# Optimization experiments

Hardware: AMD Instinct MI355X
Metric: run time of the kernel (lower is better)

Reference implementation:

```python
import jax, jax.numpy as jnp
import numpy as np

VOCAB = 32000      # embedding vocab
EMBED = 300        # nn.Embedding embedding_dim
HID = 256          # sequence_size // 2 per direction (sequence_size=512)
N_COLS = 4096      # number of columns (split-delimited segments)
SEG_LEN = 8        # 7 description words + 1 SPLIT token per column
SPLIT_IDX = 0
T = N_COLS * SEG_LEN


def setup_inputs() -> dict:
    key = jax.random.key(0)
    ks = jax.random.split(key, 10)
    # tokens in [1, VOCAB), with SPLIT_IDX at the end of every SEG_LEN block
    seq = jax.random.randint(ks[0], (T,), 1, VOCAB)
    seq = seq.at[SEG_LEN - 1::SEG_LEN].set(SPLIT_IDX)
    s = 1.0 / np.sqrt(HID)  # torch LSTM default init range

    def u(k, shape):
        return jax.random.uniform(k, shape, jnp.float32, -s, s)

    return {
        "emb_table": jax.random.normal(ks[1], (VOCAB, EMBED), jnp.float32),
        "w_ih_f": u(ks[2], (4 * HID, EMBED)),
        "w_hh_f": u(ks[3], (4 * HID, HID)),
        "b_ih_f": u(ks[4], (4 * HID,)),
        "b_hh_f": u(ks[5], (4 * HID,)),
        "w_ih_b": u(ks[6], (4 * HID, EMBED)),
        "w_hh_b": u(ks[7], (4 * HID, HID)),
        "b_ih_b": u(ks[8], (4 * HID,)),
        "b_hh_b": u(ks[9], (4 * HID,)),
        "seq_s": seq,
    }


def _run_dir(xg, mask, w_hh, reverse):
    """Masked LSTM over time. xg: [L, N, 4H] precomputed input gates (+bias),
    mask: [L, N] validity per original time index. Returns final hidden [N, H]."""
    if reverse:
        xg = xg[::-1]
        mask = mask[::-1]
    N = xg.shape[1]

    def step(carry, inp):
        h, c = carry
        g, m = inp
        gates = g + h @ w_hh.T                       # [N, 4H]
        i, f, gg, o = jnp.split(gates, 4, axis=-1)   # torch gate order i,f,g,o
        c_new = jax.nn.sigmoid(f) * c + jax.nn.sigmoid(i) * jnp.tanh(gg)
        h_new = jax.nn.sigmoid(o) * jnp.tanh(c_new)
        m = m[:, None]
        return (jnp.where(m, h_new, h), jnp.where(m, c_new, c)), None

    init = (jnp.zeros((N, HID), xg.dtype), jnp.zeros((N, HID), xg.dtype))
    (h, _), _ = jax.lax.scan(step, init, (xg, mask))
    return h


def reference(emb_table, w_ih_f, w_hh_f, b_ih_f, b_hh_f,
              w_ih_b, w_hh_b, b_ih_b, b_hh_b, seq_s):
    col = jnp.arange(N_COLS)
    # torch code: ends = nonzero(split); begins = roll(ends,1); begins[0] = 0
    # => segment i>0 starts AT the previous split token (len SEG_LEN);
    #    segment 0 is [0, SEG_LEN-1) (len SEG_LEN-1).
    begins = jnp.where(col == 0, 0, col * SEG_LEN - 1)
    lengths = jnp.where(col == 0, SEG_LEN - 1, SEG_LEN)
    idx = jnp.clip(begins[:, None] + jnp.arange(SEG_LEN)[None, :], 0, T - 1)  # [N, L]
    mask = jnp.arange(SEG_LEN)[None, :] < lengths[:, None]                    # [N, L]

    segs = emb_table[seq_s][idx]        # [N, L, E] embedded ragged segments
    x = segs.transpose(1, 0, 2)          # [L, N, E]
    m = mask.T                           # [L, N]

    xg_f = jnp.einsum('lne,ge->lng', x, w_ih_f) + b_ih_f + b_hh_f
    xg_b = jnp.einsum('lne,ge->lng', x, w_ih_b) + b_ih_b + b_hh_b
    h_f = _run_dir(xg_f, m, w_hh_f, reverse=False)   # forward final hidden
    h_b = _run_dir(xg_b, m, w_hh_b, reverse=True)    # backward final hidden (t=0)
    # torch final_hidden.view(-1) per column == concat(fwd, bwd)
    return jnp.concatenate([h_f, h_b], axis=-1)      # [N_COLS, 2*HID]
```

## Files before the change

kernel.cpp:

```cpp
#include <hip/hip_runtime.h>

typedef unsigned int uint;
typedef unsigned short ushort;
typedef __attribute__((ext_vector_type(8))) short short8;
typedef __attribute__((ext_vector_type(4))) float f32x4;
typedef __attribute__((ext_vector_type(4))) uint uint4w;

#define T_LEN 32768
#define EMB 300
#define HID 256
#define NCOLS 4096

__device__ __forceinline__ ushort f2bf(float f) {
  uint u = __float_as_uint(f);
  return (ushort)((u + 0x7fffu + ((u >> 16) & 1u)) >> 16);
}
__device__ __forceinline__ float bf2f(ushort u) {
  return __uint_as_float(((uint)u) << 16);
}
__device__ __forceinline__ float fexp2(float x) {
  float r; asm("v_exp_f32 %0, %1" : "=v"(r) : "v"(x)); return r;
}
__device__ __forceinline__ float frcp(float x) {
  float r; asm("v_rcp_f32 %0, %1" : "=v"(r) : "v"(x)); return r;
}
__device__ __forceinline__ float sigm(float x) {
  return frcp(1.f + fexp2(-1.442695041f * x));
}
__device__ __forceinline__ float tanh_(float x) {
  return 2.f * frcp(1.f + fexp2(-2.885390082f * x)) - 1.f;
}

__device__ __forceinline__ void gload_lds16(const void* g, void* l) {
  __builtin_amdgcn_global_load_lds((const __attribute__((address_space(1))) void*)g,
                                   (__attribute__((address_space(3))) void*)l, 16, 0, 0);
}

__global__ void prep_kernel(const float* __restrict__ emb,
                            const float* __restrict__ wihf, const float* __restrict__ whhf,
                            const float* __restrict__ bihf, const float* __restrict__ bhhf,
                            const float* __restrict__ wihb, const float* __restrict__ whhb,
                            const float* __restrict__ bihb, const float* __restrict__ bhhb,
                            const int* __restrict__ seq,
                            ushort* __restrict__ X, ushort* __restrict__ Wih,
                            ushort* __restrict__ Whh3, float* __restrict__ bias) {
  const int NX = T_LEN * 40;
  const int NWIH = 2048 * 40;
  const int NWHH = 2048 * 32;
  const int NB = 2048;
  const int total = NX + NWIH + NWHH + NB;
  for (int t = blockIdx.x * blockDim.x + threadIdx.x; t < total; t += gridDim.x * blockDim.x) {
    if (t < NX) {
      int r = t / 40, k8 = t % 40, k = k8 * 8;
      int col = r >> 3, j = r & 7;
      int tok = (col == 0) ? j : (col * 8 - 1 + j);
      const float* src = emb + (long)seq[tok] * EMB + k;
      alignas(16) ushort tmp[8];
#pragma unroll
      for (int i = 0; i < 8; ++i) tmp[i] = (k + i < EMB) ? f2bf(src[i]) : (ushort)0;
      *(uint4w*)(X + (long)r * 320 + k) = *(const uint4w*)tmp;
    } else if (t < NX + NWIH) {
      int t2 = t - NX;
      int n = t2 / 40, k8 = t2 % 40, k = k8 * 8;
      const float* src = ((n < 1024) ? wihf : wihb) + (long)(n & 1023) * EMB + k;
      alignas(16) ushort tmp[8];
#pragma unroll
      for (int i = 0; i < 8; ++i) tmp[i] = (k + i < EMB) ? f2bf(src[i]) : (ushort)0;
      *(uint4w*)(Wih + (long)n * 320 + k) = *(const uint4w*)tmp;
    } else if (t < NX + NWIH + NWHH) {
      int t3 = t - NX - NWIH;
      int n = t3 / 32, k8 = t3 % 32;
      int dd = n >> 10, rowg = n & 1023;
      int gp = rowg >> 9, gi = (rowg >> 8) & 1, w5 = (rowg >> 5) & 7;
      int qq = (rowg >> 4) & 1, lnn = rowg & 15;
      int ks = k8 >> 2, cc = k8 & 3, s = ks * 2 + gp;
      const float* src = ((dd == 0) ? whhf : whhb) + (long)rowg * HID + k8 * 8;
      alignas(16) ushort tmp[8];
#pragma unroll
      for (int i = 0; i < 8; ++i) tmp[i] = f2bf(src[i]);
      long didx = (((long)(dd * 16 + s)) * 8 + w5) * 2048 + cc * 512 + gi * 256 + qq * 128 + lnn * 8;
      *(uint4w*)(Whh3 + didx) = *(const uint4w*)tmp;
    } else {
      int n = t - NX - NWIH - NWHH;
      bias[n] = (n < 1024) ? (bihf[n] + bhhf[n]) : (bihb[n - 1024] + bhhb[n - 1024]);
    }
  }
}

__global__ void gemm_xg_kernel(const ushort* __restrict__ X, const ushort* __restrict__ Wih,
                               const float* __restrict__ bias, ushort* __restrict__ xg) {
  __shared__ ushort a_lds[2][256 * 32];
  const int tid = threadIdx.x;
  const int lane = tid & 63, w = tid >> 6;
  const int wr = w >> 1, wc = w & 1;
  const int qrow = lane >> 4, ln = lane & 15;
  const int m0 = blockIdx.x * 256, n0 = blockIdx.y * 128;

  auto stage = [&](int buf, int kt) {
#pragma unroll
    for (int q = 0; q < 2; ++q) {
      int byteoff = w * 2048 + q * 1024 + lane * 16;
      int row = byteoff >> 6, koff = byteoff & 63;
      const char* src = (const char*)X + (long)(m0 + row) * 640 + kt * 64 + koff;
      void* dst = (char*)&a_lds[buf][0] + w * 2048 + q * 1024;
      gload_lds16(src, dst);
    }
  };

  const ushort* wb = Wih + (long)(n0 + wc * 64 + ln) * 320 + qrow * 8;
  auto loadB = [&](short8 (&dst)[4], int kt) {
#pragma unroll
    for (int nt = 0; nt < 4; ++nt)
      dst[nt] = *(const short8*)(wb + nt * 16 * 320 + kt * 32);
  };

  const f32x4 fzero = {0.f, 0.f, 0.f, 0.f};
  f32x4 acc[4][4];
#pragma unroll
  for (int i = 0; i < 4; ++i)
#pragma unroll
    for (int jj = 0; jj < 4; ++jj) acc[i][jj] = fzero;

  auto gemmK = [&](short8 (&b)[4], int buf) {
    short8 a[4];
#pragma unroll
    for (int rt = 0; rt < 4; ++rt)
      a[rt] = *(const short8*)&a_lds[buf][(wr * 64 + rt * 16 + ln) * 32 + qrow * 8];
#pragma unroll
    for (int rt = 0; rt < 4; ++rt)
#pragma unroll
      for (int nt = 0; nt < 4; ++nt)
        acc[rt][nt] = __builtin_amdgcn_mfma_f32_16x16x32_bf16(a[rt], b[nt], acc[rt][nt], 0, 0, 0);
  };

  short8 bA[4], bB[4];
  stage(0, 0);
  loadB(bA, 0);
#pragma unroll 1
  for (int kt2 = 0; kt2 < 5; ++kt2) {
    const int kt = kt2 * 2;
    __syncthreads();
    loadB(bB, kt + 1);
    __builtin_amdgcn_sched_barrier(0);
    if (kt < 9) stage(1, kt + 1);
    __builtin_amdgcn_sched_barrier(0);
    gemmK(bA, 0);
    __syncthreads();
    if (kt2 < 4) loadB(bA, kt + 2);
    __builtin_amdgcn_sched_barrier(0);
    if (kt + 2 < 10) stage(0, kt + 2);
    __builtin_amdgcn_sched_barrier(0);
    gemmK(bB, 1);
  }

  ushort* sbuf = &a_lds[0][0];
  float bv[4];
#pragma unroll
  for (int nt = 0; nt < 4; ++nt) bv[nt] = bias[n0 + wc * 64 + nt * 16 + ln];
#pragma unroll
  for (int R = 0; R < 4; ++R) {
    __syncthreads();
#pragma unroll
    for (int nt = 0; nt < 4; ++nt)
#pragma unroll
      for (int r = 0; r < 4; ++r)
        sbuf[(wr * 16 + qrow * 4 + r) * 128 + wc * 64 + nt * 16 + ln] = f2bf(acc[R][nt][r] + bv[nt]);
    __syncthreads();
#pragma unroll
    for (int p = 0; p < 2; ++p) {
      int srow = p * 32 + (tid >> 4);
      int c0 = (tid & 15) * 8;
      uint4w v = *(uint4w*)&sbuf[srow * 128 + c0];
      *(uint4w*)&xg[(long)(m0 + (srow >> 4) * 64 + R * 16 + (srow & 15)) * 2048 + n0 + c0] = v;
    }
  }
}

__global__ __launch_bounds__(512) void lstm_kernel(const ushort* __restrict__ xg,
                                                   const ushort* __restrict__ Whh3,
                                                   float* __restrict__ out) {
  __shared__ ushort h_lds[32][264];
  __shared__ alignas(16) char b_lds[8][4][4096];
  const int tid = threadIdx.x;
  const int lane = tid & 63, w = tid >> 6;
  const int qrow = lane >> 4, ln = lane & 15;
  const int bid = blockIdx.x;
  const int d = bid >> 7, cg = bid & 127;

  const char* wsrc = (const char*)Whh3 + (((long)(d * 16) * 8 + w) << 12);
  char* wdst = &b_lds[w][0][0];

  auto stageB = [&](int s, int slot) {
    const char* src = wsrc + ((long)s << 15) + lane * 16;
    char* dst = wdst + slot * 4096;
#pragma unroll
    for (int q2 = 0; q2 < 4; ++q2) gload_lds16(src + q2 * 1024, dst + q2 * 1024);
  };

  float c_st[2][2][4], h_st[2][2][4];
#pragma unroll
  for (int rt = 0; rt < 2; ++rt)
#pragma unroll
    for (int q = 0; q < 2; ++q)
#pragma unroll
      for (int r = 0; r < 4; ++r) { c_st[rt][q][r] = 0.f; h_st[rt][q][r] = 0.f; }

  const f32x4 fzero = {0.f, 0.f, 0.f, 0.f};

#pragma unroll 1
  for (int it = 0; it < 8; ++it) {
    const int j = d ? (7 - it) : it;
    asm volatile("s_waitcnt lgkmcnt(0)" ::: "memory");
    __builtin_amdgcn_s_barrier();
    asm volatile("" ::: "memory");

    f32x4 acc[4][2][2];
#pragma unroll
    for (int g = 0; g < 4; ++g)
#pragma unroll
      for (int q = 0; q < 2; ++q)
#pragma unroll
        for (int rt = 0; rt < 2; ++rt) acc[g][q][rt] = fzero;

    if (it > 0) {
      asm volatile("s_waitcnt vmcnt(4)" ::: "memory");
      __builtin_amdgcn_sched_barrier(0);
      short8 bbuf[2][4], abuf[2][2];
      {
        const char* bb = wdst + qrow * 1024;
#pragma unroll
        for (int gi = 0; gi < 2; ++gi)
#pragma unroll
          for (int q = 0; q < 2; ++q)
            bbuf[0][gi * 2 + q] = *(const short8*)(bb + gi * 512 + q * 256 + ln * 16);
        abuf[0][0] = *(const short8*)&h_lds[ln][qrow * 8];
        abuf[0][1] = *(const short8*)&h_lds[16 + ln][qrow * 8];
      }
#pragma unroll
      for (int p = 0; p < 16; ++p) {
        const int ks = p >> 1, gp = p & 1;
        if (p < 15) {
          const char* bb = wdst + ((p + 1) & 3) * 4096 + qrow * 1024;
#pragma unroll
          for (int gi = 0; gi < 2; ++gi)
#pragma unroll
            for (int q = 0; q < 2; ++q)
              bbuf[(p + 1) & 1][gi * 2 + q] = *(const short8*)(bb + gi * 512 + q * 256 + ln * 16);
        }
        if (gp == 1 && ks < 7) {
          abuf[(ks + 1) & 1][0] = *(const short8*)&h_lds[ln][(ks + 1) * 32 + qrow * 8];
          abuf[(ks + 1) & 1][1] = *(const short8*)&h_lds[16 + ln][(ks + 1) * 32 + qrow * 8];
        }
        if (p <= 12) stageB(p + 3, (p + 3) & 3);
        if (p == 15)                 { asm volatile("s_waitcnt lgkmcnt(0)" ::: "memory"); }
        else if (gp == 1 && ks < 7)  { asm volatile("s_waitcnt lgkmcnt(6)" ::: "memory"); }
        else                         { asm volatile("s_waitcnt lgkmcnt(4)" ::: "memory"); }
        __builtin_amdgcn_sched_barrier(0);
        short8 a0 = abuf[ks & 1][0], a1 = abuf[ks & 1][1];
#pragma unroll
        for (int gi = 0; gi < 2; ++gi)
#pragma unroll
          for (int q = 0; q < 2; ++q) {
            short8 b = bbuf[p & 1][gi * 2 + q];
            const int g = gp * 2 + gi;
            acc[g][q][0] = __builtin_amdgcn_mfma_f32_16x16x32_bf16(a0, b, acc[g][q][0], 0, 0, 0);
            acc[g][q][1] = __builtin_amdgcn_mfma_f32_16x16x32_bf16(a1, b, acc[g][q][1], 0, 0, 0);
          }
        if (p < 15) { asm volatile("s_waitcnt vmcnt(4)" ::: "memory"); }
        __builtin_amdgcn_sched_barrier(0);
      }
    }

    if (it < 7) { stageB(0, 0); stageB(1, 1); stageB(2, 2); }
    __builtin_amdgcn_sched_barrier(0);

    const ushort* xgb = xg + (long)(cg * 256 + j) * 2048 + qrow * 65536 + d * 1024 + w * 32 + ln;
    ushort xv[2][2][4][4];
#pragma unroll
    for (int rt = 0; rt < 2; ++rt)
#pragma unroll
      for (int q = 0; q < 2; ++q)
#pragma unroll
        for (int r = 0; r < 4; ++r)
#pragma unroll
          for (int g = 0; g < 4; ++g)
            xv[rt][q][r][g] = xgb[(long)rt * 262144 + r * 16384 + g * 256 + q * 16];

    asm volatile("s_waitcnt lgkmcnt(0)" ::: "memory");
    __builtin_amdgcn_s_barrier();
    asm volatile("" ::: "memory");

    const bool mstep = d ? (it == 0) : (it == 7);
#pragma unroll
    for (int rt = 0; rt < 2; ++rt)
#pragma unroll
      for (int q = 0; q < 2; ++q)
#pragma unroll
        for (int r = 0; r < 4; ++r) {
          int cc = rt * 16 + qrow * 4 + r;
          int hid = w * 32 + q * 16 + ln;
          float pi = acc[0][q][rt][r] + bf2f(xv[rt][q][r][0]);
          float pf = acc[1][q][rt][r] + bf2f(xv[rt][q][r][1]);
          float pg = acc[2][q][rt][r] + bf2f(xv[rt][q][r][2]);
          float po = acc[3][q][rt][r] + bf2f(xv[rt][q][r][3]);
          float cn = sigm(pf) * c_st[rt][q][r] + sigm(pi) * tanh_(pg);
          float hn = sigm(po) * tanh_(cn);
          bool skip = mstep && (cg == 0) && (cc == 0);
          if (!skip) { c_st[rt][q][r] = cn; h_st[rt][q][r] = hn; }
          h_lds[cc][hid] = f2bf(h_st[rt][q][r]);
        }
  }

#pragma unroll
  for (int rt = 0; rt < 2; ++rt)
#pragma unroll
    for (int q = 0; q < 2; ++q)
#pragma unroll
      for (int r = 0; r < 4; ++r) {
        int cc = rt * 16 + qrow * 4 + r;
        int hid = w * 32 + q * 16 + ln;
        out[(long)(cg * 32 + cc) * 512 + d * 256 + hid] = h_st[rt][q][r];
      }
}

extern "C" void kernel_launch(void* const* d_in, const int* in_sizes, int n_in,
                              void* d_out, int out_size, void* d_ws, size_t ws_size,
                              hipStream_t stream) {
  const float* emb  = (const float*)d_in[0];
  const float* wihf = (const float*)d_in[1];
  const float* whhf = (const float*)d_in[2];
  const float* bihf = (const float*)d_in[3];
  const float* bhhf = (const float*)d_in[4];
  const float* wihb = (const float*)d_in[5];
  const float* whhb = (const float*)d_in[6];
  const float* bihb = (const float*)d_in[7];
  const float* bhhb = (const float*)d_in[8];
  const int*   seq  = (const int*)d_in[9];
  float* out = (float*)d_out;

  char* ws = (char*)d_ws;
  ushort* xg   = (ushort*)(ws);
  ushort* X    = (ushort*)(ws + 134217728);
  ushort* Wih  = (ushort*)(ws + 155189248);
  ushort* Whh3 = (ushort*)(ws + 156499968);
  float*  bias = (float*)(ws + 157548544);

  prep_kernel<<<dim3(1024), dim3(256), 0, stream>>>(emb, wihf, whhf, bihf, bhhf,
                                                    wihb, whhb, bihb, bhhb, seq,
                                                    X, Wih, Whh3, bias);
  gemm_xg_kernel<<<dim3(128, 16), dim3(512), 0, stream>>>(X, Wih, bias, xg);
  lstm_kernel<<<dim3(256), dim3(512), 0, stream>>>(xg, Whh3, out);
}
```

Before: 239.0 us.

## Restructure input-projection GEMM into triple-buffered B pipeline with single barrier per step

The input-gate GEMM's K loop is fully unrolled. B fragments are rotated through three register buffers so loads run two steps ahead, and each step uses one explicit s_barrier guarded by explicit lgkmcnt/vmcnt waits, replacing two __syncthreads per pair of steps. This aims to overlap global loads of B and LDS staging of A with the MFMA work and to cut barrier overhead. In the recurrent kernel, the tail vmcnt waits are also adjusted so the last iterations drain outstanding loads correctly. The cost is higher register pressure and reliance on hand-counted wait values being right.

```diff
diff --git a/kernel.cpp b/kernel.cpp
--- a/kernel.cpp
+++ b/kernel.cpp
@@ -133,24 +133,21 @@
         acc[rt][nt] = __builtin_amdgcn_mfma_f32_16x16x32_bf16(a[rt], b[nt], acc[rt][nt], 0, 0, 0);
   };
 
-  short8 bA[4], bB[4];
+  short8 b[3][4];
+  loadB(b[0], 0);
   stage(0, 0);
-  loadB(bA, 0);
-#pragma unroll 1
-  for (int kt2 = 0; kt2 < 5; ++kt2) {
-    const int kt = kt2 * 2;
-    __syncthreads();
-    loadB(bB, kt + 1);
+  loadB(b[1], 1);
+#pragma unroll
+  for (int kt = 0; kt < 10; ++kt) {
+    asm volatile("s_waitcnt lgkmcnt(0)" ::: "memory");
+    if (kt < 9) { asm volatile("s_waitcnt vmcnt(4)" ::: "memory"); }
+    else        { asm volatile("s_waitcnt vmcnt(0)" ::: "memory"); }
+    __builtin_amdgcn_s_barrier();
+    asm volatile("" ::: "memory");
+    if (kt < 9) stage((kt + 1) & 1, kt + 1);
+    if (kt < 8) loadB(b[(kt + 2) % 3], kt + 2);
     __builtin_amdgcn_sched_barrier(0);
-    if (kt < 9) stage(1, kt + 1);
-    __builtin_amdgcn_sched_barrier(0);
-    gemmK(bA, 0);
-    __syncthreads();
-    if (kt2 < 4) loadB(bA, kt + 2);
-    __builtin_amdgcn_sched_barrier(0);
-    if (kt + 2 < 10) stage(0, kt + 2);
-    __builtin_amdgcn_sched_barrier(0);
-    gemmK(bB, 1);
+    gemmK(b[kt % 3], kt & 1);
   }
 
   ushort* sbuf = &a_lds[0][0];
@@ -266,7 +263,8 @@
             acc[g][q][0] = __builtin_amdgcn_mfma_f32_16x16x32_bf16(a0, b, acc[g][q][0], 0, 0, 0);
             acc[g][q][1] = __builtin_amdgcn_mfma_f32_16x16x32_bf16(a1, b, acc[g][q][1], 0, 0, 0);
           }
-        if (p < 15) { asm volatile("s_waitcnt vmcnt(4)" ::: "memory"); }
+        if (p <= 12)      { asm volatile("s_waitcnt vmcnt(4)" ::: "memory"); }
+        else if (p == 13) { asm volatile("s_waitcnt vmcnt(0)" ::: "memory"); }
         __builtin_amdgcn_sched_barrier(0);
       }
     }
```

Result: slower. 355.4 us (+48.7%).

## Retile input-gate GEMM to 64x256 blocks of 256 threads and fix LSTM waitcnt tail

Applied to the files above, without the earlier changes.

Reshapes the input-projection GEMM from 256x128 tiles with 8 waves to 64x256 tiles with 4 waves, each wave covering a 64x64 output patch. The shared A buffer shrinks and launch bounds ask for 3 blocks per CU, aiming for higher occupancy and more blocks across CUs, at the cost of reloading the X rows more times per output column. The epilogue now writes 256-wide rows with two 16-byte stores per thread. In the LSTM kernel the vmcnt wait at the end of the pipelined loop is changed to drain fully at p==13 and skip waits afterwards, matching the point where staging stops.

```diff
diff --git a/kernel.cpp b/kernel.cpp
--- a/kernel.cpp
+++ b/kernel.cpp
@@ -87,27 +87,24 @@
   }
 }
 
-__global__ void gemm_xg_kernel(const ushort* __restrict__ X, const ushort* __restrict__ Wih,
-                               const float* __restrict__ bias, ushort* __restrict__ xg) {
-  __shared__ ushort a_lds[2][256 * 32];
+__global__ __launch_bounds__(256, 3) void gemm_xg_kernel(const ushort* __restrict__ X,
+                                                         const ushort* __restrict__ Wih,
+                                                         const float* __restrict__ bias,
+                                                         ushort* __restrict__ xg) {
+  __shared__ ushort a_lds[2][64 * 32];
   const int tid = threadIdx.x;
   const int lane = tid & 63, w = tid >> 6;
-  const int wr = w >> 1, wc = w & 1;
   const int qrow = lane >> 4, ln = lane & 15;
-  const int m0 = blockIdx.x * 256, n0 = blockIdx.y * 128;
+  const int m0 = blockIdx.x * 64, n0 = blockIdx.y * 256;
 
   auto stage = [&](int buf, int kt) {
-#pragma unroll
-    for (int q = 0; q < 2; ++q) {
-      int byteoff = w * 2048 + q * 1024 + lane * 16;
-      int row = byteoff >> 6, koff = byteoff & 63;
-      const char* src = (const char*)X + (long)(m0 + row) * 640 + kt * 64 + koff;
-      void* dst = (char*)&a_lds[buf][0] + w * 2048 + q * 1024;
-      gload_lds16(src, dst);
-    }
+    int row = tid >> 2, koff = (tid & 3) * 16;
+    const char* src = (const char*)X + (long)(m0 + row) * 640 + kt * 64 + koff;
+    void* dst = (char*)&a_lds[buf][0] + w * 1024;
+    gload_lds16(src, dst);
   };
 
-  const ushort* wb = Wih + (long)(n0 + wc * 64 + ln) * 320 + qrow * 8;
+  const ushort* wb = Wih + (long)(n0 + w * 64 + ln) * 320 + qrow * 8;
   auto loadB = [&](short8 (&dst)[4], int kt) {
 #pragma unroll
     for (int nt = 0; nt < 4; ++nt)
@@ -125,7 +122,7 @@
     short8 a[4];
 #pragma unroll
     for (int rt = 0; rt < 4; ++rt)
-      a[rt] = *(const short8*)&a_lds[buf][(wr * 64 + rt * 16 + ln) * 32 + qrow * 8];
+      a[rt] = *(const short8*)&a_lds[buf][(rt * 16 + ln) * 32 + qrow * 8];
 #pragma unroll
     for (int rt = 0; rt < 4; ++rt)
 #pragma unroll
@@ -156,7 +153,7 @@
   ushort* sbuf = &a_lds[0][0];
   float bv[4];
 #pragma unroll
-  for (int nt = 0; nt < 4; ++nt) bv[nt] = bias[n0 + wc * 64 + nt * 16 + ln];
+  for (int nt = 0; nt < 4; ++nt) bv[nt] = bias[n0 + w * 64 + nt * 16 + ln];
 #pragma unroll
   for (int R = 0; R < 4; ++R) {
     __syncthreads();
@@ -164,15 +161,15 @@
     for (int nt = 0; nt < 4; ++nt)
 #pragma unroll
       for (int r = 0; r < 4; ++r)
-        sbuf[(wr * 16 + qrow * 4 + r) * 128 + wc * 64 + nt * 16 + ln] = f2bf(acc[R][nt][r] + bv[nt]);
+        sbuf[(qrow * 4 + r) * 256 + w * 64 + nt * 16 + ln] = f2bf(acc[R][nt][r] + bv[nt]);
     __syncthreads();
-#pragma unroll
-    for (int p = 0; p < 2; ++p) {
-      int srow = p * 32 + (tid >> 4);
-      int c0 = (tid & 15) * 8;
-      uint4w v = *(uint4w*)&sbuf[srow * 128 + c0];
-      *(uint4w*)&xg[(long)(m0 + (srow >> 4) * 64 + R * 16 + (srow & 15)) * 2048 + n0 + c0] = v;
-    }
+    int srow = tid >> 4;
+    int c0 = (tid & 15) * 16;
+    uint4w v0 = *(uint4w*)&sbuf[srow * 256 + c0];
+    uint4w v1 = *(uint4w*)&sbuf[srow * 256 + c0 + 8];
+    ushort* gdst = &xg[(long)(m0 + R * 16 + srow) * 2048 + n0 + c0];
+    *(uint4w*)gdst = v0;
+    *(uint4w*)(gdst + 8) = v1;
   }
 }
 
@@ -266,7 +263,8 @@
             acc[g][q][0] = __builtin_amdgcn_mfma_f32_16x16x32_bf16(a0, b, acc[g][q][0], 0, 0, 0);
             acc[g][q][1] = __builtin_amdgcn_mfma_f32_16x16x32_bf16(a1, b, acc[g][q][1], 0, 0, 0);
           }
-        if (p < 15) { asm volatile("s_waitcnt vmcnt(4)" ::: "memory"); }
+        if (p <= 12)      { asm volatile("s_waitcnt vmcnt(4)" ::: "memory"); }
+        else if (p == 13) { asm volatile("s_waitcnt vmcnt(0)" ::: "memory"); }
         __builtin_amdgcn_sched_barrier(0);
       }
     }
@@ -348,6 +346,6 @@
   prep_kernel<<<dim3(1024), dim3(256), 0, stream>>>(emb, wihf, whhf, bihf, bhhf,
                                                     wihb, whhb, bihb, bhhb, seq,
                                                     X, Wih, Whh3, bias);
-  gemm_xg_kernel<<<dim3(128, 16), dim3(512), 0, stream>>>(X, Wih, bias, xg);
+  gemm_xg_kernel<<<dim3(512, 8), dim3(256), 0, stream>>>(X, Wih, bias, xg);
   lstm_kernel<<<dim3(256), dim3(512), 0, stream>>>(xg, Whh3, out);
 }
```

Measured after the change: 237.4 us (median of 2 runs). About the same (-0.7%).
